# Performance work log

Measured on AMD Instinct MI355X. Metric: run time of the kernel, lower is better.

The kernel has to match this reference:

```python
import jax, jax.numpy as jnp
import numpy as np

NEG = -100.0
M2M, M2I, M2D, I2M, I2I, D2M, D2D = range(7)
LOG_Q = float(np.log(0.25))


def _d_chain(fM, aM2D, aD2D):
    """Sequential delete-state recurrence along motif axis k.
    fD[k] = logaddexp(aM2D[k-1] + fM[k-1], aD2D[k-1] + fD[k-1]), fD[0] = NEG.
    fM: (B, K+1); aM2D, aD2D: (B, K+1). Returns (B, K+1)."""
    B, Kp1 = fM.shape
    K = Kp1 - 1

    def step(fd_prev, inp):
        am, ad, fm = inp  # each (B,)
        fd = jnp.logaddexp(am + fm, ad + fd_prev)
        return fd, fd

    init = jnp.full((B,), NEG, dtype=fM.dtype)
    _, fds = jax.lax.scan(step, init, (aM2D[:, :K].T, aD2D[:, :K].T, fM[:, :K].T))
    return jnp.concatenate([init[:, None], fds.T], axis=1)


def _profile_hmm_loss(a, e, x):
    """pHMM forward algorithm (log-space). a: (B,K+1,7), e: (B,K,4), x: (B,L) int.
    Returns -log P(x) per batch element, shape (B,)."""
    B, Kp1, _ = a.shape
    K = Kp1 - 1

    fM0 = jnp.full((B, Kp1), NEG, dtype=a.dtype).at[:, 0].set(0.0)
    fI0 = jnp.full((B, Kp1), NEG, dtype=a.dtype)
    fD0 = _d_chain(fM0, a[:, :, M2D], a[:, :, D2D])

    def l_step(carry, x_l):
        fM, fI, fD = carry
        # emission for symbol x_l at each match state k: (B, K)
        esel = jnp.take_along_axis(e, x_l[:, None, None].astype(jnp.int32), axis=2)[:, :, 0]
        prev = jnp.logaddexp(
            jnp.logaddexp(a[:, :K, M2M] + fM[:, :K], a[:, :K, I2M] + fI[:, :K]),
            a[:, :K, D2M] + fD[:, :K],
        )
        fM_new = jnp.concatenate([jnp.full((B, 1), NEG, dtype=a.dtype), esel + prev], axis=1)
        fI_new = LOG_Q + jnp.logaddexp(a[:, :, M2I] + fM, a[:, :, I2I] + fI)
        fD_new = _d_chain(fM_new, a[:, :, M2D], a[:, :, D2D])
        return (fM_new, fI_new, fD_new), None

    (fM, fI, fD), _ = jax.lax.scan(l_step, (fM0, fI0, fD0), x.T)

    final = jnp.stack(
        [fM[:, K] + a[:, K, M2M], fI[:, K] + a[:, K, I2M], fD[:, K] + a[:, K, D2M]],
        axis=1,
    )
    return -jax.nn.logsumexp(final, axis=1)


def _kld_loss(mus, logvars):
    return -0.5 * jnp.sum(1.0 + logvars - mus * mus - jnp.exp(logvars), axis=1)


def setup_inputs() -> dict:
    key = jax.random.key(0)
    k1, k2, k3, k4, k5 = jax.random.split(key, 5)
    B, K, L, E = 4096, 64, 128, 16
    batch_input = jax.random.randint(k1, (B, L), 0, 4, dtype=jnp.int32)
    transition_probs = jax.random.normal(k2, (B, K + 1, 7), dtype=jnp.float32)
    emission_probs = jax.random.normal(k3, (B, K, 4), dtype=jnp.float32)
    mus = jax.random.normal(k4, (B, E), dtype=jnp.float32)
    logvars = jax.random.normal(k5, (B, E), dtype=jnp.float32)
    return {
        "batch_input": batch_input,
        "transition_probs": transition_probs,
        "emission_probs": emission_probs,
        "mus": mus,
        "logvars": logvars,
    }


def reference(batch_input, transition_probs, emission_probs, mus, logvars):
    beta = 1.0
    recon = jnp.mean(_profile_hmm_loss(transition_probs, emission_probs, batch_input))
    kld = jnp.mean(_kld_loss(mus, logvars))
    return recon + beta * kld
```

## Files before the change

kernel.cpp:

```cpp
#include <hip/hip_runtime.h>
#include <math.h>


namespace {

constexpr float kLog2e = 1.4426950408889634f;
constexpr float kLn2   = 0.6931471805599453f;

__device__ __forceinline__ float fexp(float x) {
    return __builtin_amdgcn_exp2f(x * kLog2e);
}

__device__ __forceinline__ float rfl(float x) {
    return __builtin_bit_cast(float,
        __builtin_amdgcn_readfirstlane(__builtin_bit_cast(int, x)));
}

template <int CTRL, bool BC>
__device__ __forceinline__ float dppf(float old, float src) {
    int r = __builtin_amdgcn_update_dpp(__builtin_bit_cast(int, old),
                                        __builtin_bit_cast(int, src),
                                        CTRL, 0xF, 0xF, BC);
    return __builtin_bit_cast(float, r);
}

__global__ __launch_bounds__(256) void phmm_vae_kernel(
    const int* __restrict__ xg,
    const float* __restrict__ ag,
    const float* __restrict__ eg,
    const float* __restrict__ mug,
    const float* __restrict__ lvg,
    float* __restrict__ out, int B)
{
    const int tid  = threadIdx.x;
    const int lane = tid & 63;
    const int wv   = tid >> 6;
    const int b    = (blockIdx.x << 2) + wv;

    __shared__ float2 ec[4][4][64];
    __shared__ float part[4];
    float contrib = 0.0f;

    if (b < B) {
        const float* ab = ag + (size_t)b * (65 * 7);
        const float* eb = eg + (size_t)b * (64 * 4);
        const int*   xb = xg + (size_t)b * 128;

        const int j = lane;
        const float a2  = ab[j * 7 + 2];
        const float a6  = ab[j * 7 + 6];
        const float a5  = ab[(j + 1) * 7 + 5];
        const float A1M2M  = fexp(ab[(j + 1) * 7 + 0]);
        const float QA1M2I = 0.25f * fexp(ab[(j + 1) * 7 + 1]);
        const float A1I2M  = fexp(ab[(j + 1) * 7 + 3]);
        const float QA1I2I = 0.25f * fexp(ab[(j + 1) * 7 + 4]);
        const float A0M2M = fexp(ab[0]);
        const float D0f   = rfl(0.25f * fexp(ab[4]));
        const float G0f   = rfl(0.25f * fexp(ab[3] + ab[1] - ab[0]));

        float4 ev = *reinterpret_cast<const float4*>(eb + j * 4);
        const float E0 = fexp(ev.x), E1 = fexp(ev.y);
        const float E2 = fexp(ev.z), E3 = fexp(ev.w);

        const int xlo = xb[lane];
        const int xhi = xb[64 + lane];
        const unsigned long long b0lo = __ballot(xlo & 1);
        const unsigned long long b1lo = __ballot(xlo & 2);
        const unsigned long long b0hi = __ballot(xhi & 1);
        const unsigned long long b1hi = __ballot(xhi & 2);

        const float a5p = dppf<0x138, false>(0.0f, a5);
        const float dh  = fexp(a6 + a5 - a5p);
        const float wM2D = fexp(a2 + a5);
        const float C0 = wM2D * dppf<0x138, false>(0.0f, E0);
        const float C1 = wM2D * dppf<0x138, false>(0.0f, E1);
        const float C2 = wM2D * dppf<0x138, false>(0.0f, E2);
        const float C3 = wM2D * dppf<0x138, false>(0.0f, E3);

        ec[wv][0][lane] = make_float2(E0, C0);
        ec[wv][1][lane] = make_float2(E1, C1);
        ec[wv][2][lane] = make_float2(E2, C2);
        ec[wv][3][lane] = make_float2(E3, C3);

        const float V1 = dh;
        const float V2 = V1 * dppf<0x111, false>(1.0f, V1);
        const float V4 = V2 * dppf<0x112, false>(1.0f, V2);
        const float V8 = V4 * dppf<0x114, false>(1.0f, V4);
        const float V1m = (lane >= 1)  ? V1 : 0.0f;
        const float V2m = (lane >= 2)  ? V2 : 0.0f;
        const float V4m = (lane >= 4)  ? V4 : 0.0f;
        const float V8m = (lane >= 8)  ? V8 : 0.0f;
        float Q = dh;
        Q *= dppf<0x111, false>(1.0f, Q);
        Q *= dppf<0x112, false>(1.0f, Q);
        Q *= dppf<0x114, false>(1.0f, Q);
        Q *= dppf<0x118, false>(1.0f, Q);
        const int   row = lane >> 4;
        const float Q47 = __shfl(Q, 47, 64);
        const float QmA = (row == 1 || row == 3) ? Q : 0.0f;
        const float QmB = (row == 2) ? Q : ((row == 3) ? Q * Q47 : 0.0f);

        auto scan_asm = [&](float prev, float Cs) -> float {
            float y;
            asm("s_nop 1\n\t"
                "v_mul_f32_dpp %0, %1, %2 wave_shr:1 row_mask:0xf bank_mask:0xf bound_ctrl:0\n\t"
                "s_nop 1\n\t"
                "v_fmac_f32_dpp %0, %0, %3 row_shr:1 row_mask:0xf bank_mask:0xf bound_ctrl:0\n\t"
                "s_nop 1\n\t"
                "v_fmac_f32_dpp %0, %0, %4 row_shr:2 row_mask:0xf bank_mask:0xf bound_ctrl:0\n\t"
                "s_nop 1\n\t"
                "v_fmac_f32_dpp %0, %0, %5 row_shr:4 row_mask:0xf bank_mask:0xf bound_ctrl:0\n\t"
                "s_nop 1\n\t"
                "v_fmac_f32_dpp %0, %0, %6 row_shr:8 row_mask:0xf bank_mask:0xf bound_ctrl:0\n\t"
                "s_nop 1\n\t"
                "v_fmac_f32_dpp %0, %0, %7 row_bcast:15 row_mask:0xf bank_mask:0xf bound_ctrl:0\n\t"
                "s_nop 1\n\t"
                "v_fmac_f32_dpp %0, %0, %8 row_bcast:31 row_mask:0xf bank_mask:0xf bound_ctrl:0"
                : "=&v"(y)
                : "v"(prev), "v"(Cs), "v"(V1m), "v"(V2m), "v"(V4m), "v"(V8m),
                  "v"(QmA), "v"(QmB));
            return y;
        };

        float y0 = (lane == 0) ? wM2D : 0.0f;
        y0 = fmaf(V1m, dppf<0x111, true>(0.0f, y0), y0);
        y0 = fmaf(V2m, dppf<0x112, true>(0.0f, y0), y0);
        y0 = fmaf(V4m, dppf<0x114, true>(0.0f, y0), y0);
        y0 = fmaf(V8m, dppf<0x118, true>(0.0f, y0), y0);
        y0 = fmaf(QmA, dppf<0x142, true>(0.0f, y0), y0);
        y0 = fmaf(QmB, dppf<0x143, true>(0.0f, y0), y0);

        float fM = 0.0f, fI = 0.0f;
        float pl = y0;
        float p0v = A0M2M;
        float LS = 0.0f;

        auto sym_of = [&](int l) -> unsigned {
            const unsigned long long m0 = ((l & 64) == 0) ? b0lo : b0hi;
            const unsigned long long m1 = ((l & 64) == 0) ? b1lo : b1hi;
            const int sh = l & 63;
            return (unsigned)((m0 >> sh) & 1ull) |
                   ((unsigned)((m1 >> sh) & 1ull) << 1);
        };

        float2 EC0 = ec[wv][sym_of(0)][lane];
        float2 EC1 = ec[wv][sym_of(1)][lane];

#pragma unroll 8
        for (int l = 0; l < 128; ++l) {
            float2 EC2 = ec[wv][sym_of((l + 2) & 127)][lane];

            const float prev = dppf<0x138, false>(p0v, pl);
            const float fMn = EC0.x * prev;
            const float z = scan_asm(prev, EC0.y);
            fI = fmaf(QA1M2I, fM, QA1I2I * fI);
            fM = fMn;
            pl = fmaf(A1M2M, fM, fmaf(A1I2M, fI, z));
            p0v *= (l == 0) ? G0f : D0f;

            if ((l & 7) == 7) {
                float m = fmaxf(fmaxf(fM, fI), pl);
                m = fmaxf(m, dppf<0xB1,  true>(0.0f, m));
                m = fmaxf(m, dppf<0x4E,  true>(0.0f, m));
                m = fmaxf(m, dppf<0x141, true>(0.0f, m));
                m = fmaxf(m, dppf<0x140, true>(0.0f, m));
                m = fmaxf(m, 1e-35f);
                int mb = __builtin_bit_cast(int, m);
                unsigned u0 = (unsigned)__builtin_amdgcn_readlane(mb, 0);
                unsigned u1 = (unsigned)__builtin_amdgcn_readlane(mb, 16);
                unsigned u2 = (unsigned)__builtin_amdgcn_readlane(mb, 32);
                unsigned u3 = (unsigned)__builtin_amdgcn_readlane(mb, 48);
                unsigned ua = u0 > u1 ? u0 : u1;
                unsigned ub = u2 > u3 ? u2 : u3;
                unsigned um = ua > ub ? ua : ub;
                int ee = (int)(um >> 23);
                float r = __builtin_bit_cast(float, (unsigned)(254 - ee) << 23);
                LS += (float)(ee - 127);
                fM *= r; fI *= r; pl *= r; p0v *= r;
            }

            EC0 = EC1;
            EC1 = EC2;
        }

        const float Fv = __shfl(pl, 63, 64);
        const float loss = -(__builtin_amdgcn_logf(Fv) + LS) * kLn2;

        float kt = 0.0f;
        if (lane < 16) {
            float mu = mug[(size_t)b * 16 + lane];
            float lv = lvg[(size_t)b * 16 + lane];
            kt = 1.0f + lv - mu * mu - fexp(lv);
        }
        kt += __shfl_xor(kt, 1, 64);
        kt += __shfl_xor(kt, 2, 64);
        kt += __shfl_xor(kt, 4, 64);
        kt += __shfl_xor(kt, 8, 64);
        float kldb = __shfl(-0.5f * kt, 0, 64);

        contrib = (loss + kldb) * (1.0f / 4096.0f);
    }

    if (lane == 63) part[wv] = (b < B) ? contrib : 0.0f;
    __syncthreads();
    if (tid == 0) {
        atomicAdd(out, part[0] + part[1] + part[2] + part[3]);
    }
}

}

extern "C" void kernel_launch(void* const* d_in, const int* in_sizes, int n_in,
                              void* d_out, int out_size, void* d_ws, size_t ws_size,
                              hipStream_t stream) {
    const int*   x  = (const int*)d_in[0];
    const float* a  = (const float*)d_in[1];
    const float* e  = (const float*)d_in[2];
    const float* mu = (const float*)d_in[3];
    const float* lv = (const float*)d_in[4];
    float* out = (float*)d_out;

    const int B = in_sizes[0] / 128;
    const int grid = (B + 3) / 4;

    phmm_vae_kernel<<<grid, 256, 0, stream>>>(x, a, e, mu, lv, out, B);
}
```

Before: 93.18 us.

## Replace per-step delete-chain DPP scan with anti-diagonal wavefront recurrence

The old kernel resolved the sequential delete-state chain inside every time step with a seven-stage DPP prefix scan. The new kernel sweeps the DP grid along anti-diagonals over 191 steps, so each lane needs only a single shifted neighbour value per step, and lanes past the sequence end are zeroed at renormalisation points. Emissions are packed as bf16 pairs in registers and selected with v_perm, which removes the LDS table. This trades the long per-step DPP dependency chain for more iterations and reduced emission precision, and it adds a clamp on the insert seed.

```diff
diff --git a/kernel.cpp b/kernel.cpp
--- a/kernel.cpp
+++ b/kernel.cpp
@@ -11,7 +11,7 @@
     return __builtin_amdgcn_exp2f(x * kLog2e);
 }
 
-__device__ __forceinline__ float rfl(float x) {
+__device__ __forceinline__ float rflf(float x) {
     return __builtin_bit_cast(float,
         __builtin_amdgcn_readfirstlane(__builtin_bit_cast(int, x)));
 }
@@ -22,6 +22,10 @@
                                         __builtin_bit_cast(int, src),
                                         CTRL, 0xF, 0xF, BC);
     return __builtin_bit_cast(float, r);
+}
+
+__device__ __forceinline__ int dpp_shr1_i(int old, int src) {
+    return __builtin_amdgcn_update_dpp(old, src, 0x138, 0xF, 0xF, false);
 }
 
 __global__ __launch_bounds__(256) void phmm_vae_kernel(
@@ -37,7 +41,6 @@
     const int wv   = tid >> 6;
     const int b    = (blockIdx.x << 2) + wv;
 
-    __shared__ float2 ec[4][4][64];
     __shared__ float part[4];
     float contrib = 0.0f;
 
@@ -47,20 +50,26 @@
         const int*   xb = xg + (size_t)b * 128;
 
         const int j = lane;
-        const float a2  = ab[j * 7 + 2];
-        const float a6  = ab[j * 7 + 6];
-        const float a5  = ab[(j + 1) * 7 + 5];
-        const float A1M2M  = fexp(ab[(j + 1) * 7 + 0]);
-        const float QA1M2I = 0.25f * fexp(ab[(j + 1) * 7 + 1]);
-        const float A1I2M  = fexp(ab[(j + 1) * 7 + 3]);
-        const float QA1I2I = 0.25f * fexp(ab[(j + 1) * 7 + 4]);
-        const float A0M2M = fexp(ab[0]);
-        const float D0f   = rfl(0.25f * fexp(ab[4]));
-        const float G0f   = rfl(0.25f * fexp(ab[3] + ab[1] - ab[0]));
+        const float M2Mc = fexp(ab[j * 7 + 0]);
+        const float M2Dc = fexp(ab[j * 7 + 2]);
+        const float I2Mc = fexp(ab[j * 7 + 3]);
+        const float D2Mc = fexp(ab[j * 7 + 5]);
+        const float D2Dc = fexp(ab[j * 7 + 6]);
+        const float QM2I = 0.25f * fexp(ab[(j + 1) * 7 + 1]);
+        const float QI2I = 0.25f * fexp(ab[(j + 1) * 7 + 4]);
+        const float A64M2M = fexp(ab[64 * 7 + 0]);
+        const float A64I2M = fexp(ab[64 * 7 + 3]);
+        const float A64D2M = fexp(ab[64 * 7 + 5]);
+        const float G0f = rflf(0.25f * fexp(ab[1]));
+        const float D0f = rflf(0.25f * fexp(ab[4]));
 
         float4 ev = *reinterpret_cast<const float4*>(eb + j * 4);
-        const float E0 = fexp(ev.x), E1 = fexp(ev.y);
-        const float E2 = fexp(ev.z), E3 = fexp(ev.w);
+        auto bfr = [](float x) -> unsigned {
+            unsigned u = __builtin_bit_cast(unsigned, x);
+            return (u + 0x8000u) >> 16;
+        };
+        const unsigned E10 = (bfr(fexp(ev.y)) << 16) | bfr(fexp(ev.x));
+        const unsigned E32 = (bfr(fexp(ev.w)) << 16) | bfr(fexp(ev.z));
 
         const int xlo = xb[lane];
         const int xhi = xb[64 + lane];
@@ -69,97 +78,44 @@
         const unsigned long long b0hi = __ballot(xhi & 1);
         const unsigned long long b1hi = __ballot(xhi & 2);
 
-        const float a5p = dppf<0x138, false>(0.0f, a5);
-        const float dh  = fexp(a6 + a5 - a5p);
-        const float wM2D = fexp(a2 + a5);
-        const float C0 = wM2D * dppf<0x138, false>(0.0f, E0);
-        const float C1 = wM2D * dppf<0x138, false>(0.0f, E1);
-        const float C2 = wM2D * dppf<0x138, false>(0.0f, E2);
-        const float C3 = wM2D * dppf<0x138, false>(0.0f, E3);
-
-        ec[wv][0][lane] = make_float2(E0, C0);
-        ec[wv][1][lane] = make_float2(E1, C1);
-        ec[wv][2][lane] = make_float2(E2, C2);
-        ec[wv][3][lane] = make_float2(E3, C3);
-
-        const float V1 = dh;
-        const float V2 = V1 * dppf<0x111, false>(1.0f, V1);
-        const float V4 = V2 * dppf<0x112, false>(1.0f, V2);
-        const float V8 = V4 * dppf<0x114, false>(1.0f, V4);
-        const float V1m = (lane >= 1)  ? V1 : 0.0f;
-        const float V2m = (lane >= 2)  ? V2 : 0.0f;
-        const float V4m = (lane >= 4)  ? V4 : 0.0f;
-        const float V8m = (lane >= 8)  ? V8 : 0.0f;
-        float Q = dh;
-        Q *= dppf<0x111, false>(1.0f, Q);
-        Q *= dppf<0x112, false>(1.0f, Q);
-        Q *= dppf<0x114, false>(1.0f, Q);
-        Q *= dppf<0x118, false>(1.0f, Q);
-        const int   row = lane >> 4;
-        const float Q47 = __shfl(Q, 47, 64);
-        const float QmA = (row == 1 || row == 3) ? Q : 0.0f;
-        const float QmB = (row == 2) ? Q : ((row == 3) ? Q * Q47 : 0.0f);
-
-        auto scan_asm = [&](float prev, float Cs) -> float {
-            float y;
-            asm("s_nop 1\n\t"
-                "v_mul_f32_dpp %0, %1, %2 wave_shr:1 row_mask:0xf bank_mask:0xf bound_ctrl:0\n\t"
-                "s_nop 1\n\t"
-                "v_fmac_f32_dpp %0, %0, %3 row_shr:1 row_mask:0xf bank_mask:0xf bound_ctrl:0\n\t"
-                "s_nop 1\n\t"
-                "v_fmac_f32_dpp %0, %0, %4 row_shr:2 row_mask:0xf bank_mask:0xf bound_ctrl:0\n\t"
-                "s_nop 1\n\t"
-                "v_fmac_f32_dpp %0, %0, %5 row_shr:4 row_mask:0xf bank_mask:0xf bound_ctrl:0\n\t"
-                "s_nop 1\n\t"
-                "v_fmac_f32_dpp %0, %0, %6 row_shr:8 row_mask:0xf bank_mask:0xf bound_ctrl:0\n\t"
-                "s_nop 1\n\t"
-                "v_fmac_f32_dpp %0, %0, %7 row_bcast:15 row_mask:0xf bank_mask:0xf bound_ctrl:0\n\t"
-                "s_nop 1\n\t"
-                "v_fmac_f32_dpp %0, %0, %8 row_bcast:31 row_mask:0xf bank_mask:0xf bound_ctrl:0"
-                : "=&v"(y)
-                : "v"(prev), "v"(Cs), "v"(V1m), "v"(V2m), "v"(V4m), "v"(V8m),
-                  "v"(QmA), "v"(QmB));
-            return y;
+        auto sel_of = [&](int idx) -> int {
+            const unsigned long long m0 = (idx & 64) ? b0hi : b0lo;
+            const unsigned long long m1 = (idx & 64) ? b1hi : b1lo;
+            const int sh = idx & 63;
+            unsigned s = (unsigned)((m0 >> sh) & 1ull) |
+                         ((unsigned)((m1 >> sh) & 1ull) << 1);
+            return (int)(0x00000C0Cu + s * 0x02020000u + 0x01000000u);
         };
 
-        float y0 = (lane == 0) ? wM2D : 0.0f;
-        y0 = fmaf(V1m, dppf<0x111, true>(0.0f, y0), y0);
-        y0 = fmaf(V2m, dppf<0x112, true>(0.0f, y0), y0);
-        y0 = fmaf(V4m, dppf<0x114, true>(0.0f, y0), y0);
-        y0 = fmaf(V8m, dppf<0x118, true>(0.0f, y0), y0);
-        y0 = fmaf(QmA, dppf<0x142, true>(0.0f, y0), y0);
-        y0 = fmaf(QmB, dppf<0x143, true>(0.0f, y0), y0);
-
         float fM = 0.0f, fI = 0.0f;
-        float pl = y0;
-        float p0v = A0M2M;
+        float fD = (lane == 0) ? M2Dc : 0.0f;
+        float pM = (lane == 0) ? 1.0f : 0.0f;
+        float pI = 0.0f, pD = 0.0f;
+        float p0I = G0f;
+        int selreg = sel_of(0);
         float LS = 0.0f;
 
-        auto sym_of = [&](int l) -> unsigned {
-            const unsigned long long m0 = ((l & 64) == 0) ? b0lo : b0hi;
-            const unsigned long long m1 = ((l & 64) == 0) ? b1lo : b1hi;
-            const int sh = l & 63;
-            return (unsigned)((m0 >> sh) & 1ull) |
-                   ((unsigned)((m1 >> sh) & 1ull) << 1);
-        };
+#pragma unroll 8
+        for (int t = 1; t <= 191; ++t) {
+            const float Es = __builtin_bit_cast(float,
+                __builtin_amdgcn_perm(E32, E10, (unsigned)selreg));
 
-        float2 EC0 = ec[wv][sym_of(0)][lane];
-        float2 EC1 = ec[wv][sym_of(1)][lane];
+            const float sM = dppf<0x138, false>(0.0f, fM);
+            const float sI = dppf<0x138, false>(p0I,  fI);
+            const float sD = dppf<0x138, true >(0.0f, fD);
 
-#pragma unroll 8
-        for (int l = 0; l < 128; ++l) {
-            float2 EC2 = ec[wv][sym_of((l + 2) & 127)][lane];
+            fI = fmaf(QM2I, fM, QI2I * fI);
+            const float fMn = Es * fmaf(M2Mc, pM, fmaf(I2Mc, pI, D2Mc * pD));
+            fD = fmaf(M2Dc, sM, D2Dc * sD);
+            fM = fMn;
+            pM = sM; pI = sI; pD = sD;
+            p0I *= D0f;
+            selreg = dpp_shr1_i(sel_of(t & 127), selreg);
 
-            const float prev = dppf<0x138, false>(p0v, pl);
-            const float fMn = EC0.x * prev;
-            const float z = scan_asm(prev, EC0.y);
-            fI = fmaf(QA1M2I, fM, QA1I2I * fI);
-            fM = fMn;
-            pl = fmaf(A1M2M, fM, fmaf(A1I2M, fI, z));
-            p0v *= (l == 0) ? G0f : D0f;
-
-            if ((l & 7) == 7) {
-                float m = fmaxf(fmaxf(fM, fI), pl);
+            if ((t & 7) == 0) {
+                const int thr = t - 128;
+                if (lane < thr) { fM = 0.0f; fI = 0.0f; fD = 0.0f; }
+                float m = fmaxf(fmaxf(fM, fI), fD);
                 m = fmaxf(m, dppf<0xB1,  true>(0.0f, m));
                 m = fmaxf(m, dppf<0x4E,  true>(0.0f, m));
                 m = fmaxf(m, dppf<0x141, true>(0.0f, m));
@@ -176,15 +132,20 @@
                 int ee = (int)(um >> 23);
                 float r = __builtin_bit_cast(float, (unsigned)(254 - ee) << 23);
                 LS += (float)(ee - 127);
-                fM *= r; fI *= r; pl *= r; p0v *= r;
+                fM *= r; fI *= r; fD *= r;
+                pM *= r; pI *= r; pD *= r;
+                p0I = fminf(p0I * r, 1e18f);
             }
-
-            EC0 = EC1;
-            EC1 = EC2;
         }
 
-        const float Fv = __shfl(pl, 63, 64);
-        const float loss = -(__builtin_amdgcn_logf(Fv) + LS) * kLn2;
+        const float FM = rflf(__builtin_bit_cast(float,
+            __builtin_amdgcn_readlane(__builtin_bit_cast(int, fM), 63)));
+        const float FI = __builtin_bit_cast(float,
+            __builtin_amdgcn_readlane(__builtin_bit_cast(int, fI), 63));
+        const float FD = __builtin_bit_cast(float,
+            __builtin_amdgcn_readlane(__builtin_bit_cast(int, fD), 63));
+        const float F = fmaf(A64M2M, FM, fmaf(A64I2M, FI, A64D2M * FD));
+        const float loss = -(__builtin_amdgcn_logf(F) + LS) * kLn2;
 
         float kt = 0.0f;
         if (lane < 16) {
```

New measurement: 110.6 us. +18.7%, slower.

## Process two batch elements per wavefront to interleave dependent DPP scan chains

Applied to the files above, without the earlier changes.

Each wavefront now runs the forward recurrence for two batch elements at once. Their DPP prefix-scan instructions are interleaved in one asm block, so the s_nop hazard padding shrinks and independent work fills the latency of each dependent DPP step. The cost is half as many blocks, higher register pressure, and a guard that requires both elements to be in range (drops a trailing element when B is odd). With B=4096 the grid halves to 512 blocks, which may leave some CUs underused.

```diff
diff --git a/kernel.cpp b/kernel.cpp
--- a/kernel.cpp
+++ b/kernel.cpp
@@ -11,7 +11,7 @@
     return __builtin_amdgcn_exp2f(x * kLog2e);
 }
 
-__device__ __forceinline__ float rfl(float x) {
+__device__ __forceinline__ float rflf(float x) {
     return __builtin_bit_cast(float,
         __builtin_amdgcn_readfirstlane(__builtin_bit_cast(int, x)));
 }
@@ -22,6 +22,116 @@
                                         __builtin_bit_cast(int, src),
                                         CTRL, 0xF, 0xF, BC);
     return __builtin_bit_cast(float, r);
+}
+
+struct ES {
+    float A1M2M, QA1M2I, A1I2M, QA1I2I;
+    float V1m, V2m, V4m, V8m, QmA, QmB;
+    float D0f, G0f;
+    float fM, fI, pl, p0v, LS;
+    unsigned long long b0lo, b1lo, b0hi, b1hi;
+};
+
+__device__ __forceinline__ void setup_elem(
+    ES& S, const float* __restrict__ ab, const float* __restrict__ eb,
+    const int* __restrict__ xb, float2* __restrict__ ecs ,
+    int lane)
+{
+    const int j = lane;
+    const float a2 = ab[j * 7 + 2];
+    const float a6 = ab[j * 7 + 6];
+    const float a5 = ab[(j + 1) * 7 + 5];
+    S.A1M2M  = fexp(ab[(j + 1) * 7 + 0]);
+    S.QA1M2I = 0.25f * fexp(ab[(j + 1) * 7 + 1]);
+    S.A1I2M  = fexp(ab[(j + 1) * 7 + 3]);
+    S.QA1I2I = 0.25f * fexp(ab[(j + 1) * 7 + 4]);
+    const float A0M2M = fexp(ab[0]);
+    S.D0f = rflf(0.25f * fexp(ab[4]));
+    S.G0f = rflf(0.25f * fexp(ab[3] + ab[1] - ab[0]));
+
+    float4 ev = *reinterpret_cast<const float4*>(eb + j * 4);
+    const float E0 = fexp(ev.x), E1 = fexp(ev.y);
+    const float E2 = fexp(ev.z), E3 = fexp(ev.w);
+
+    const int xlo = xb[lane];
+    const int xhi = xb[64 + lane];
+    S.b0lo = __ballot(xlo & 1);
+    S.b1lo = __ballot(xlo & 2);
+    S.b0hi = __ballot(xhi & 1);
+    S.b1hi = __ballot(xhi & 2);
+
+    const float a5p = dppf<0x138, false>(0.0f, a5);
+    const float dh  = fexp(a6 + a5 - a5p);
+    const float wM2D = fexp(a2 + a5);
+    const float C0 = wM2D * dppf<0x138, false>(0.0f, E0);
+    const float C1 = wM2D * dppf<0x138, false>(0.0f, E1);
+    const float C2 = wM2D * dppf<0x138, false>(0.0f, E2);
+    const float C3 = wM2D * dppf<0x138, false>(0.0f, E3);
+
+    ecs[0 * 64 + lane] = make_float2(E0, C0);
+    ecs[1 * 64 + lane] = make_float2(E1, C1);
+    ecs[2 * 64 + lane] = make_float2(E2, C2);
+    ecs[3 * 64 + lane] = make_float2(E3, C3);
+
+    const float V1 = dh;
+    const float V2 = V1 * dppf<0x111, false>(1.0f, V1);
+    const float V4 = V2 * dppf<0x112, false>(1.0f, V2);
+    const float V8 = V4 * dppf<0x114, false>(1.0f, V4);
+    S.V1m = (lane >= 1)  ? V1 : 0.0f;
+    S.V2m = (lane >= 2)  ? V2 : 0.0f;
+    S.V4m = (lane >= 4)  ? V4 : 0.0f;
+    S.V8m = (lane >= 8)  ? V8 : 0.0f;
+    float Q = dh;
+    Q *= dppf<0x111, false>(1.0f, Q);
+    Q *= dppf<0x112, false>(1.0f, Q);
+    Q *= dppf<0x114, false>(1.0f, Q);
+    Q *= dppf<0x118, false>(1.0f, Q);
+    const int   row = lane >> 4;
+    const float Q47 = __shfl(Q, 47, 64);
+    S.QmA = (row == 1 || row == 3) ? Q : 0.0f;
+    S.QmB = (row == 2) ? Q : ((row == 3) ? Q * Q47 : 0.0f);
+
+    float y0 = (lane == 0) ? wM2D : 0.0f;
+    y0 = fmaf(S.V1m, dppf<0x111, true>(0.0f, y0), y0);
+    y0 = fmaf(S.V2m, dppf<0x112, true>(0.0f, y0), y0);
+    y0 = fmaf(S.V4m, dppf<0x114, true>(0.0f, y0), y0);
+    y0 = fmaf(S.V8m, dppf<0x118, true>(0.0f, y0), y0);
+    y0 = fmaf(S.QmA, dppf<0x142, true>(0.0f, y0), y0);
+    y0 = fmaf(S.QmB, dppf<0x143, true>(0.0f, y0), y0);
+
+    S.fM = 0.0f; S.fI = 0.0f;
+    S.pl = y0;
+    S.p0v = A0M2M;
+    S.LS = 0.0f;
+}
+
+__device__ __forceinline__ unsigned sym_of(const ES& S, int l) {
+    const unsigned long long m0 = ((l & 64) == 0) ? S.b0lo : S.b0hi;
+    const unsigned long long m1 = ((l & 64) == 0) ? S.b1lo : S.b1hi;
+    const int sh = l & 63;
+    return (unsigned)((m0 >> sh) & 1ull) |
+           ((unsigned)((m1 >> sh) & 1ull) << 1);
+}
+
+__device__ __forceinline__ void rescale(ES& S) {
+    float m = fmaxf(fmaxf(S.fM, S.fI), S.pl);
+    m = fmaxf(m, dppf<0xB1,  true>(0.0f, m));
+    m = fmaxf(m, dppf<0x4E,  true>(0.0f, m));
+    m = fmaxf(m, dppf<0x141, true>(0.0f, m));
+    m = fmaxf(m, dppf<0x140, true>(0.0f, m));
+    m = fmaxf(m, 1e-35f);
+    int mb = __builtin_bit_cast(int, m);
+    unsigned u0 = (unsigned)__builtin_amdgcn_readlane(mb, 0);
+    unsigned u1 = (unsigned)__builtin_amdgcn_readlane(mb, 16);
+    unsigned u2 = (unsigned)__builtin_amdgcn_readlane(mb, 32);
+    unsigned u3 = (unsigned)__builtin_amdgcn_readlane(mb, 48);
+    unsigned ua = u0 > u1 ? u0 : u1;
+    unsigned ub = u2 > u3 ? u2 : u3;
+    unsigned um = ua > ub ? ua : ub;
+    int ee = (int)(um >> 23);
+    float r = __builtin_bit_cast(float, (unsigned)(254 - ee) << 23);
+    S.LS += (float)(ee - 127);
+    S.fM *= r; S.fI *= r; S.pl *= r; S.p0v *= r;
 }
 
 __global__ __launch_bounds__(256) void phmm_vae_kernel(
@@ -35,173 +145,107 @@
     const int tid  = threadIdx.x;
     const int lane = tid & 63;
     const int wv   = tid >> 6;
-    const int b    = (blockIdx.x << 2) + wv;
-
-    __shared__ float2 ec[4][4][64];
+    const int bA   = (blockIdx.x << 3) + (wv << 1);
+    const int bB   = bA + 1;
+
+    __shared__ float2 ec[4][2][4][64];
     __shared__ float part[4];
     float contrib = 0.0f;
 
-    if (b < B) {
-        const float* ab = ag + (size_t)b * (65 * 7);
-        const float* eb = eg + (size_t)b * (64 * 4);
-        const int*   xb = xg + (size_t)b * 128;
-
-        const int j = lane;
-        const float a2  = ab[j * 7 + 2];
-        const float a6  = ab[j * 7 + 6];
-        const float a5  = ab[(j + 1) * 7 + 5];
-        const float A1M2M  = fexp(ab[(j + 1) * 7 + 0]);
-        const float QA1M2I = 0.25f * fexp(ab[(j + 1) * 7 + 1]);
-        const float A1I2M  = fexp(ab[(j + 1) * 7 + 3]);
-        const float QA1I2I = 0.25f * fexp(ab[(j + 1) * 7 + 4]);
-        const float A0M2M = fexp(ab[0]);
-        const float D0f   = rfl(0.25f * fexp(ab[4]));
-        const float G0f   = rfl(0.25f * fexp(ab[3] + ab[1] - ab[0]));
-
-        float4 ev = *reinterpret_cast<const float4*>(eb + j * 4);
-        const float E0 = fexp(ev.x), E1 = fexp(ev.y);
-        const float E2 = fexp(ev.z), E3 = fexp(ev.w);
-
-        const int xlo = xb[lane];
-        const int xhi = xb[64 + lane];
-        const unsigned long long b0lo = __ballot(xlo & 1);
-        const unsigned long long b1lo = __ballot(xlo & 2);
-        const unsigned long long b0hi = __ballot(xhi & 1);
-        const unsigned long long b1hi = __ballot(xhi & 2);
-
-        const float a5p = dppf<0x138, false>(0.0f, a5);
-        const float dh  = fexp(a6 + a5 - a5p);
-        const float wM2D = fexp(a2 + a5);
-        const float C0 = wM2D * dppf<0x138, false>(0.0f, E0);
-        const float C1 = wM2D * dppf<0x138, false>(0.0f, E1);
-        const float C2 = wM2D * dppf<0x138, false>(0.0f, E2);
-        const float C3 = wM2D * dppf<0x138, false>(0.0f, E3);
-
-        ec[wv][0][lane] = make_float2(E0, C0);
-        ec[wv][1][lane] = make_float2(E1, C1);
-        ec[wv][2][lane] = make_float2(E2, C2);
-        ec[wv][3][lane] = make_float2(E3, C3);
-
-        const float V1 = dh;
-        const float V2 = V1 * dppf<0x111, false>(1.0f, V1);
-        const float V4 = V2 * dppf<0x112, false>(1.0f, V2);
-        const float V8 = V4 * dppf<0x114, false>(1.0f, V4);
-        const float V1m = (lane >= 1)  ? V1 : 0.0f;
-        const float V2m = (lane >= 2)  ? V2 : 0.0f;
-        const float V4m = (lane >= 4)  ? V4 : 0.0f;
-        const float V8m = (lane >= 8)  ? V8 : 0.0f;
-        float Q = dh;
-        Q *= dppf<0x111, false>(1.0f, Q);
-        Q *= dppf<0x112, false>(1.0f, Q);
-        Q *= dppf<0x114, false>(1.0f, Q);
-        Q *= dppf<0x118, false>(1.0f, Q);
-        const int   row = lane >> 4;
-        const float Q47 = __shfl(Q, 47, 64);
-        const float QmA = (row == 1 || row == 3) ? Q : 0.0f;
-        const float QmB = (row == 2) ? Q : ((row == 3) ? Q * Q47 : 0.0f);
-
-        auto scan_asm = [&](float prev, float Cs) -> float {
-            float y;
-            asm("s_nop 1\n\t"
-                "v_mul_f32_dpp %0, %1, %2 wave_shr:1 row_mask:0xf bank_mask:0xf bound_ctrl:0\n\t"
-                "s_nop 1\n\t"
-                "v_fmac_f32_dpp %0, %0, %3 row_shr:1 row_mask:0xf bank_mask:0xf bound_ctrl:0\n\t"
-                "s_nop 1\n\t"
-                "v_fmac_f32_dpp %0, %0, %4 row_shr:2 row_mask:0xf bank_mask:0xf bound_ctrl:0\n\t"
-                "s_nop 1\n\t"
-                "v_fmac_f32_dpp %0, %0, %5 row_shr:4 row_mask:0xf bank_mask:0xf bound_ctrl:0\n\t"
-                "s_nop 1\n\t"
-                "v_fmac_f32_dpp %0, %0, %6 row_shr:8 row_mask:0xf bank_mask:0xf bound_ctrl:0\n\t"
-                "s_nop 1\n\t"
-                "v_fmac_f32_dpp %0, %0, %7 row_bcast:15 row_mask:0xf bank_mask:0xf bound_ctrl:0\n\t"
-                "s_nop 1\n\t"
-                "v_fmac_f32_dpp %0, %0, %8 row_bcast:31 row_mask:0xf bank_mask:0xf bound_ctrl:0"
-                : "=&v"(y)
-                : "v"(prev), "v"(Cs), "v"(V1m), "v"(V2m), "v"(V4m), "v"(V8m),
-                  "v"(QmA), "v"(QmB));
-            return y;
-        };
-
-        float y0 = (lane == 0) ? wM2D : 0.0f;
-        y0 = fmaf(V1m, dppf<0x111, true>(0.0f, y0), y0);
-        y0 = fmaf(V2m, dppf<0x112, true>(0.0f, y0), y0);
-        y0 = fmaf(V4m, dppf<0x114, true>(0.0f, y0), y0);
-        y0 = fmaf(V8m, dppf<0x118, true>(0.0f, y0), y0);
-        y0 = fmaf(QmA, dppf<0x142, true>(0.0f, y0), y0);
-        y0 = fmaf(QmB, dppf<0x143, true>(0.0f, y0), y0);
-
-        float fM = 0.0f, fI = 0.0f;
-        float pl = y0;
-        float p0v = A0M2M;
-        float LS = 0.0f;
-
-        auto sym_of = [&](int l) -> unsigned {
-            const unsigned long long m0 = ((l & 64) == 0) ? b0lo : b0hi;
-            const unsigned long long m1 = ((l & 64) == 0) ? b1lo : b1hi;
-            const int sh = l & 63;
-            return (unsigned)((m0 >> sh) & 1ull) |
-                   ((unsigned)((m1 >> sh) & 1ull) << 1);
-        };
-
-        float2 EC0 = ec[wv][sym_of(0)][lane];
-        float2 EC1 = ec[wv][sym_of(1)][lane];
+    if (bB < B) {
+        ES SA, SB;
+        setup_elem(SA, ag + (size_t)bA * 455, eg + (size_t)bA * 256,
+                   xg + (size_t)bA * 128, &ec[wv][0][0][0], lane);
+        setup_elem(SB, ag + (size_t)bB * 455, eg + (size_t)bB * 256,
+                   xg + (size_t)bB * 128, &ec[wv][1][0][0], lane);
+        float2* ecA = &ec[wv][0][0][0];
+        float2* ecB = &ec[wv][1][0][0];
+
+        float2 ECA0 = ecA[sym_of(SA, 0) * 64 + lane];
+        float2 ECA1 = ecA[sym_of(SA, 1) * 64 + lane];
+        float2 ECB0 = ecB[sym_of(SB, 0) * 64 + lane];
+        float2 ECB1 = ecB[sym_of(SB, 1) * 64 + lane];
 
 #pragma unroll 8
         for (int l = 0; l < 128; ++l) {
-            float2 EC2 = ec[wv][sym_of((l + 2) & 127)][lane];
-
-            const float prev = dppf<0x138, false>(p0v, pl);
-            const float fMn = EC0.x * prev;
-            const float z = scan_asm(prev, EC0.y);
-            fI = fmaf(QA1M2I, fM, QA1I2I * fI);
-            fM = fMn;
-            pl = fmaf(A1M2M, fM, fmaf(A1I2M, fI, z));
-            p0v *= (l == 0) ? G0f : D0f;
-
-            if ((l & 7) == 7) {
-                float m = fmaxf(fmaxf(fM, fI), pl);
-                m = fmaxf(m, dppf<0xB1,  true>(0.0f, m));
-                m = fmaxf(m, dppf<0x4E,  true>(0.0f, m));
-                m = fmaxf(m, dppf<0x141, true>(0.0f, m));
-                m = fmaxf(m, dppf<0x140, true>(0.0f, m));
-                m = fmaxf(m, 1e-35f);
-                int mb = __builtin_bit_cast(int, m);
-                unsigned u0 = (unsigned)__builtin_amdgcn_readlane(mb, 0);
-                unsigned u1 = (unsigned)__builtin_amdgcn_readlane(mb, 16);
-                unsigned u2 = (unsigned)__builtin_amdgcn_readlane(mb, 32);
-                unsigned u3 = (unsigned)__builtin_amdgcn_readlane(mb, 48);
-                unsigned ua = u0 > u1 ? u0 : u1;
-                unsigned ub = u2 > u3 ? u2 : u3;
-                unsigned um = ua > ub ? ua : ub;
-                int ee = (int)(um >> 23);
-                float r = __builtin_bit_cast(float, (unsigned)(254 - ee) << 23);
-                LS += (float)(ee - 127);
-                fM *= r; fI *= r; pl *= r; p0v *= r;
-            }
-
-            EC0 = EC1;
-            EC1 = EC2;
+            float2 ECA2 = ecA[sym_of(SA, (l + 2) & 127) * 64 + lane];
+            float2 ECB2 = ecB[sym_of(SB, (l + 2) & 127) * 64 + lane];
+
+            const float prevA = dppf<0x138, false>(SA.p0v, SA.pl);
+            const float prevB = dppf<0x138, false>(SB.p0v, SB.pl);
+            const float fMnA = ECA0.x * prevA;
+            const float fMnB = ECB0.x * prevB;
+
+            float yA, yB;
+            asm("s_nop 1\n\t"
+                "v_mul_f32_dpp %0, %2, %3 wave_shr:1 row_mask:0xf bank_mask:0xf bound_ctrl:0\n\t"
+                "v_mul_f32_dpp %1, %4, %5 wave_shr:1 row_mask:0xf bank_mask:0xf bound_ctrl:0\n\t"
+                "s_nop 0\n\t"
+                "v_fmac_f32_dpp %0, %0, %6 row_shr:1 row_mask:0xf bank_mask:0xf bound_ctrl:0\n\t"
+                "v_fmac_f32_dpp %1, %1, %12 row_shr:1 row_mask:0xf bank_mask:0xf bound_ctrl:0\n\t"
+                "s_nop 0\n\t"
+                "v_fmac_f32_dpp %0, %0, %7 row_shr:2 row_mask:0xf bank_mask:0xf bound_ctrl:0\n\t"
+                "v_fmac_f32_dpp %1, %1, %13 row_shr:2 row_mask:0xf bank_mask:0xf bound_ctrl:0\n\t"
+                "s_nop 0\n\t"
+                "v_fmac_f32_dpp %0, %0, %8 row_shr:4 row_mask:0xf bank_mask:0xf bound_ctrl:0\n\t"
+                "v_fmac_f32_dpp %1, %1, %14 row_shr:4 row_mask:0xf bank_mask:0xf bound_ctrl:0\n\t"
+                "s_nop 0\n\t"
+                "v_fmac_f32_dpp %0, %0, %9 row_shr:8 row_mask:0xf bank_mask:0xf bound_ctrl:0\n\t"
+                "v_fmac_f32_dpp %1, %1, %15 row_shr:8 row_mask:0xf bank_mask:0xf bound_ctrl:0\n\t"
+                "s_nop 0\n\t"
+                "v_fmac_f32_dpp %0, %0, %10 row_bcast:15 row_mask:0xf bank_mask:0xf bound_ctrl:0\n\t"
+                "v_fmac_f32_dpp %1, %1, %16 row_bcast:15 row_mask:0xf bank_mask:0xf bound_ctrl:0\n\t"
+                "s_nop 0\n\t"
+                "v_fmac_f32_dpp %0, %0, %11 row_bcast:31 row_mask:0xf bank_mask:0xf bound_ctrl:0\n\t"
+                "v_fmac_f32_dpp %1, %1, %17 row_bcast:31 row_mask:0xf bank_mask:0xf bound_ctrl:0"
+                : "=&v"(yA), "=&v"(yB)
+                : "v"(prevA), "v"(ECA0.y), "v"(prevB), "v"(ECB0.y),
+                  "v"(SA.V1m), "v"(SA.V2m), "v"(SA.V4m), "v"(SA.V8m),
+                  "v"(SA.QmA), "v"(SA.QmB),
+                  "v"(SB.V1m), "v"(SB.V2m), "v"(SB.V4m), "v"(SB.V8m),
+                  "v"(SB.QmA), "v"(SB.QmB));
+
+            SA.fI = fmaf(SA.QA1M2I, SA.fM, SA.QA1I2I * SA.fI);
+            SB.fI = fmaf(SB.QA1M2I, SB.fM, SB.QA1I2I * SB.fI);
+            SA.fM = fMnA;
+            SB.fM = fMnB;
+            SA.pl = fmaf(SA.A1M2M, SA.fM, fmaf(SA.A1I2M, SA.fI, yA));
+            SB.pl = fmaf(SB.A1M2M, SB.fM, fmaf(SB.A1I2M, SB.fI, yB));
+            SA.p0v *= (l == 0) ? SA.G0f : SA.D0f;
+            SB.p0v *= (l == 0) ? SB.G0f : SB.D0f;
+
+            if ((l & 7) == 7) { rescale(SA); rescale(SB); }
+
+            ECA0 = ECA1; ECA1 = ECA2;
+            ECB0 = ECB1; ECB1 = ECB2;
         }
 
-        const float Fv = __shfl(pl, 63, 64);
-        const float loss = -(__builtin_amdgcn_logf(Fv) + LS) * kLn2;
+        const float FvA = __shfl(SA.pl, 63, 64);
+        const float FvB = __shfl(SB.pl, 63, 64);
+        const float lossA = -(__builtin_amdgcn_logf(FvA) + SA.LS) * kLn2;
+        const float lossB = -(__builtin_amdgcn_logf(FvB) + SB.LS) * kLn2;
 
         float kt = 0.0f;
         if (lane < 16) {
-            float mu = mug[(size_t)b * 16 + lane];
-            float lv = lvg[(size_t)b * 16 + lane];
+            float mu = mug[(size_t)bA * 16 + lane];
+            float lv = lvg[(size_t)bA * 16 + lane];
+            kt = 1.0f + lv - mu * mu - fexp(lv);
+        } else if (lane < 32) {
+            float mu = mug[(size_t)bB * 16 + (lane - 16)];
+            float lv = lvg[(size_t)bB * 16 + (lane - 16)];
             kt = 1.0f + lv - mu * mu - fexp(lv);
         }
         kt += __shfl_xor(kt, 1, 64);
         kt += __shfl_xor(kt, 2, 64);
         kt += __shfl_xor(kt, 4, 64);
         kt += __shfl_xor(kt, 8, 64);
-        float kldb = __shfl(-0.5f * kt, 0, 64);
-
-        contrib = (loss + kldb) * (1.0f / 4096.0f);
+        const float kldA = -0.5f * __shfl(kt, 0, 64);
+        const float kldB = -0.5f * __shfl(kt, 16, 64);
+
+        contrib = (lossA + kldA + lossB + kldB) * (1.0f / 4096.0f);
     }
 
-    if (lane == 63) part[wv] = (b < B) ? contrib : 0.0f;
+    if (lane == 63) part[wv] = (bB < B) ? contrib : 0.0f;
     __syncthreads();
     if (tid == 0) {
         atomicAdd(out, part[0] + part[1] + part[2] + part[3]);
@@ -221,7 +265,7 @@
     float* out = (float*)d_out;
 
     const int B = in_sizes[0] / 128;
-    const int grid = (B + 3) / 4;
+    const int grid = (B + 7) / 8;
 
     phmm_vae_kernel<<<grid, 256, 0, stream>>>(x, a, e, mu, lv, out, B);
 }
```

Measured after the change: 93.80 us. No clear change (+0.7%).

## Keep emissions as packed bf16 in registers and hand-schedule the step in asm

Applied to the files above, without the earlier changes.

Replaces the per-step shared-memory lookup of emission and delete-chain coefficients with bf16-packed registers selected by v_perm using a scalar selector derived from the ballot masks. The whole recurrence step becomes one inline asm block, so the independent insert and scale updates fill the DPP hazard slots of the delete-state scan. This removes LDS traffic and the wait counts on it. In exchange the emission factors are rounded to bf16, which reduces accuracy.

```diff
diff --git a/kernel.cpp b/kernel.cpp
--- a/kernel.cpp
+++ b/kernel.cpp
@@ -11,7 +11,7 @@
     return __builtin_amdgcn_exp2f(x * kLog2e);
 }
 
-__device__ __forceinline__ float rfl(float x) {
+__device__ __forceinline__ float rflf(float x) {
     return __builtin_bit_cast(float,
         __builtin_amdgcn_readfirstlane(__builtin_bit_cast(int, x)));
 }
@@ -37,26 +37,25 @@
     const int wv   = tid >> 6;
     const int b    = (blockIdx.x << 2) + wv;
 
-    __shared__ float2 ec[4][4][64];
     __shared__ float part[4];
     float contrib = 0.0f;
 
     if (b < B) {
-        const float* ab = ag + (size_t)b * (65 * 7);
-        const float* eb = eg + (size_t)b * (64 * 4);
+        const float* ab = ag + (size_t)b * 455;
+        const float* eb = eg + (size_t)b * 256;
         const int*   xb = xg + (size_t)b * 128;
 
         const int j = lane;
-        const float a2  = ab[j * 7 + 2];
-        const float a6  = ab[j * 7 + 6];
-        const float a5  = ab[(j + 1) * 7 + 5];
+        const float a2 = ab[j * 7 + 2];
+        const float a6 = ab[j * 7 + 6];
+        const float a5 = ab[(j + 1) * 7 + 5];
         const float A1M2M  = fexp(ab[(j + 1) * 7 + 0]);
         const float QA1M2I = 0.25f * fexp(ab[(j + 1) * 7 + 1]);
         const float A1I2M  = fexp(ab[(j + 1) * 7 + 3]);
         const float QA1I2I = 0.25f * fexp(ab[(j + 1) * 7 + 4]);
         const float A0M2M = fexp(ab[0]);
-        const float D0f   = rfl(0.25f * fexp(ab[4]));
-        const float G0f   = rfl(0.25f * fexp(ab[3] + ab[1] - ab[0]));
+        const float D0f = rflf(0.25f * fexp(ab[4]));
+        const float G0f = rflf(0.25f * fexp(ab[3] + ab[1] - ab[0]));
 
         float4 ev = *reinterpret_cast<const float4*>(eb + j * 4);
         const float E0 = fexp(ev.x), E1 = fexp(ev.y);
@@ -72,15 +71,19 @@
         const float a5p = dppf<0x138, false>(0.0f, a5);
         const float dh  = fexp(a6 + a5 - a5p);
         const float wM2D = fexp(a2 + a5);
-        const float C0 = wM2D * dppf<0x138, false>(0.0f, E0);
-        const float C1 = wM2D * dppf<0x138, false>(0.0f, E1);
-        const float C2 = wM2D * dppf<0x138, false>(0.0f, E2);
-        const float C3 = wM2D * dppf<0x138, false>(0.0f, E3);
-
-        ec[wv][0][lane] = make_float2(E0, C0);
-        ec[wv][1][lane] = make_float2(E1, C1);
-        ec[wv][2][lane] = make_float2(E2, C2);
-        ec[wv][3][lane] = make_float2(E3, C3);
+        const float Cf0 = wM2D * dppf<0x138, false>(0.0f, E0);
+        const float Cf1 = wM2D * dppf<0x138, false>(0.0f, E1);
+        const float Cf2 = wM2D * dppf<0x138, false>(0.0f, E2);
+        const float Cf3 = wM2D * dppf<0x138, false>(0.0f, E3);
+
+        auto bfr = [](float x) -> unsigned {
+            unsigned u = __builtin_bit_cast(unsigned, x);
+            return (u + 0x8000u) >> 16;
+        };
+        const int E10 = (int)((bfr(E1) << 16) | bfr(E0));
+        const int E32 = (int)((bfr(E3) << 16) | bfr(E2));
+        const int C10 = (int)((bfr(Cf1) << 16) | bfr(Cf0));
+        const int C32 = (int)((bfr(Cf3) << 16) | bfr(Cf2));
 
         const float V1 = dh;
         const float V2 = V1 * dppf<0x111, false>(1.0f, V1);
@@ -100,28 +103,6 @@
         const float QmA = (row == 1 || row == 3) ? Q : 0.0f;
         const float QmB = (row == 2) ? Q : ((row == 3) ? Q * Q47 : 0.0f);
 
-        auto scan_asm = [&](float prev, float Cs) -> float {
-            float y;
-            asm("s_nop 1\n\t"
-                "v_mul_f32_dpp %0, %1, %2 wave_shr:1 row_mask:0xf bank_mask:0xf bound_ctrl:0\n\t"
-                "s_nop 1\n\t"
-                "v_fmac_f32_dpp %0, %0, %3 row_shr:1 row_mask:0xf bank_mask:0xf bound_ctrl:0\n\t"
-                "s_nop 1\n\t"
-                "v_fmac_f32_dpp %0, %0, %4 row_shr:2 row_mask:0xf bank_mask:0xf bound_ctrl:0\n\t"
-                "s_nop 1\n\t"
-                "v_fmac_f32_dpp %0, %0, %5 row_shr:4 row_mask:0xf bank_mask:0xf bound_ctrl:0\n\t"
-                "s_nop 1\n\t"
-                "v_fmac_f32_dpp %0, %0, %6 row_shr:8 row_mask:0xf bank_mask:0xf bound_ctrl:0\n\t"
-                "s_nop 1\n\t"
-                "v_fmac_f32_dpp %0, %0, %7 row_bcast:15 row_mask:0xf bank_mask:0xf bound_ctrl:0\n\t"
-                "s_nop 1\n\t"
-                "v_fmac_f32_dpp %0, %0, %8 row_bcast:31 row_mask:0xf bank_mask:0xf bound_ctrl:0"
-                : "=&v"(y)
-                : "v"(prev), "v"(Cs), "v"(V1m), "v"(V2m), "v"(V4m), "v"(V8m),
-                  "v"(QmA), "v"(QmB));
-            return y;
-        };
-
         float y0 = (lane == 0) ? wM2D : 0.0f;
         y0 = fmaf(V1m, dppf<0x111, true>(0.0f, y0), y0);
         y0 = fmaf(V2m, dppf<0x112, true>(0.0f, y0), y0);
@@ -130,33 +111,68 @@
         y0 = fmaf(QmA, dppf<0x142, true>(0.0f, y0), y0);
         y0 = fmaf(QmB, dppf<0x143, true>(0.0f, y0), y0);
 
+        auto sel_of = [&](int l) -> int {
+            const unsigned long long m0 = (l & 64) ? b0hi : b0lo;
+            const unsigned long long m1 = (l & 64) ? b1hi : b1lo;
+            const int sh = l & 63;
+            unsigned s = (unsigned)((m0 >> sh) & 1ull) |
+                         ((unsigned)((m1 >> sh) & 1ull) << 1);
+            return (int)(0x00000C0Cu + s * 0x02020000u + 0x01000000u);
+        };
+
         float fM = 0.0f, fI = 0.0f;
         float pl = y0;
-        float p0v = A0M2M;
+        float p0 = A0M2M;
         float LS = 0.0f;
 
-        auto sym_of = [&](int l) -> unsigned {
-            const unsigned long long m0 = ((l & 64) == 0) ? b0lo : b0hi;
-            const unsigned long long m1 = ((l & 64) == 0) ? b1lo : b1hi;
-            const int sh = l & 63;
-            return (unsigned)((m0 >> sh) & 1ull) |
-                   ((unsigned)((m1 >> sh) & 1ull) << 1);
-        };
-
-        float2 EC0 = ec[wv][sym_of(0)][lane];
-        float2 EC1 = ec[wv][sym_of(1)][lane];
+        const int sel0 = sel_of(0);
+        float E = __builtin_bit_cast(float,
+            __builtin_amdgcn_perm((unsigned)E32, (unsigned)E10, (unsigned)sel0));
+        float C = __builtin_bit_cast(float,
+            __builtin_amdgcn_perm((unsigned)C32, (unsigned)C10, (unsigned)sel0));
 
 #pragma unroll 8
         for (int l = 0; l < 128; ++l) {
-            float2 EC2 = ec[wv][sym_of((l + 2) & 127)][lane];
-
-            const float prev = dppf<0x138, false>(p0v, pl);
-            const float fMn = EC0.x * prev;
-            const float z = scan_asm(prev, EC0.y);
-            fI = fmaf(QA1M2I, fM, QA1I2I * fI);
-            fM = fMn;
-            pl = fmaf(A1M2M, fM, fmaf(A1I2M, fI, z));
-            p0v *= (l == 0) ? G0f : D0f;
+            const int seln = sel_of((l + 1) & 127);
+            const float mul_s = (l == 0) ? G0f : D0f;
+
+            float y, pv, En, Cn;
+            asm("v_mul_f32 %[fI], %[QI2I], %[fI]\n\t"
+                "v_mov_b32 %[pv], %[p0]\n\t"
+                "v_perm_b32 %[En], %[e32], %[e10], %[sel]\n\t"
+                "v_perm_b32 %[Cn], %[c32], %[c10], %[sel]\n\t"
+                "v_mov_b32_dpp %[pv], %[pl] wave_shr:1 row_mask:0xf bank_mask:0xf\n\t"
+                "v_fmac_f32 %[fI], %[QM2I], %[fM]\n\t"
+                "v_mul_f32 %[p0], %[mul], %[p0]\n\t"
+                "v_mul_f32_dpp %[y], %[pv], %[C] wave_shr:1 row_mask:0xf bank_mask:0xf bound_ctrl:0\n\t"
+                "v_mul_f32 %[fM], %[E], %[pv]\n\t"
+                "s_nop 0\n\t"
+                "v_fmac_f32_dpp %[y], %[y], %[V1] row_shr:1 row_mask:0xf bank_mask:0xf bound_ctrl:0\n\t"
+                "s_nop 1\n\t"
+                "v_fmac_f32_dpp %[y], %[y], %[V2] row_shr:2 row_mask:0xf bank_mask:0xf bound_ctrl:0\n\t"
+                "s_nop 1\n\t"
+                "v_fmac_f32_dpp %[y], %[y], %[V4] row_shr:4 row_mask:0xf bank_mask:0xf bound_ctrl:0\n\t"
+                "s_nop 1\n\t"
+                "v_fmac_f32_dpp %[y], %[y], %[V8] row_shr:8 row_mask:0xf bank_mask:0xf bound_ctrl:0\n\t"
+                "s_nop 1\n\t"
+                "v_fmac_f32_dpp %[y], %[y], %[QmA] row_bcast:15 row_mask:0xf bank_mask:0xf bound_ctrl:0\n\t"
+                "s_nop 1\n\t"
+                "v_fmac_f32_dpp %[y], %[y], %[QmB] row_bcast:31 row_mask:0xf bank_mask:0xf bound_ctrl:0\n\t"
+                "v_fmac_f32 %[y], %[I2M], %[fI]\n\t"
+                "v_fmac_f32 %[y], %[M2M], %[fM]"
+                : [y] "=&v"(y), [pv] "=&v"(pv), [En] "=&v"(En), [Cn] "=&v"(Cn),
+                  [fM] "+v"(fM), [fI] "+v"(fI), [p0] "+v"(p0)
+                : [pl] "v"(pl), [E] "v"(E), [C] "v"(C),
+                  [e32] "v"(E32), [e10] "v"(E10),
+                  [c32] "v"(C32), [c10] "v"(C10),
+                  [V1] "v"(V1m), [V2] "v"(V2m), [V4] "v"(V4m), [V8] "v"(V8m),
+                  [QmA] "v"(QmA), [QmB] "v"(QmB),
+                  [QI2I] "v"(QA1I2I), [QM2I] "v"(QA1M2I),
+                  [I2M] "v"(A1I2M), [M2M] "v"(A1M2M),
+                  [sel] "s"(seln), [mul] "s"(mul_s));
+            pl = y;
+            E = En;
+            C = Cn;
 
             if ((l & 7) == 7) {
                 float m = fmaxf(fmaxf(fM, fI), pl);
@@ -176,11 +192,8 @@
                 int ee = (int)(um >> 23);
                 float r = __builtin_bit_cast(float, (unsigned)(254 - ee) << 23);
                 LS += (float)(ee - 127);
-                fM *= r; fI *= r; pl *= r; p0v *= r;
+                fM *= r; fI *= r; pl *= r; p0 *= r;
             }
-
-            EC0 = EC1;
-            EC1 = EC2;
         }
 
         const float Fv = __shfl(pl, 63, 64);
```

New measurement: 94.76 us. About the same (+1.7%).
